# Performance work log

Hardware: AMD Instinct MI355X
Metric: run time of the kernel (lower is better)

Reference implementation:

```python
import jax, jax.numpy as jnp
import numpy as np

N_NODES = 80000
N_EDGES = 1280000
IN_CH = 128
HID = 64
N_GRAPHS = 64
DROPOUT_P = 0.3


def setup_inputs() -> dict:
    key = jax.random.key(0)
    ks = jax.random.split(key, 12)
    x = jax.random.normal(ks[0], (N_NODES, IN_CH), dtype=jnp.float32)
    edge_index = jax.random.randint(ks[1], (2, N_EDGES), 0, N_NODES, dtype=jnp.int64 if jax.config.read('jax_enable_x64') else jnp.int32)
    batch = jnp.sort(jax.random.randint(ks[2], (N_NODES,), 0, N_GRAPHS))
    def lin(k, fan_in, fan_out):
        lim = 1.0 / np.sqrt(fan_in)
        kw, kb = jax.random.split(k)
        W = jax.random.uniform(kw, (fan_in, fan_out), minval=-lim, maxval=lim, dtype=jnp.float32)
        b = jax.random.uniform(kb, (fan_out,), minval=-lim, maxval=lim, dtype=jnp.float32)
        return W, b
    W1, b1 = lin(ks[3], IN_CH, HID)
    W2, b2 = lin(ks[4], HID, HID)
    W3, b3 = lin(ks[5], HID, HID)
    Wm1, bm1 = lin(ks[6], HID, HID)
    Wm2, bm2 = lin(ks[7], HID, 1)
    return {"x": x, "edge_index": edge_index, "batch": batch,
            "W1": W1, "b1": b1, "W2": W2, "b2": b2, "W3": W3, "b3": b3,
            "Wm1": Wm1, "bm1": bm1, "Wm2": Wm2, "bm2": bm2}


def _gcn_conv(x, W, b, src, dst, deg_inv_sqrt):
    # PyG GCNConv: h = X W; add self-loops; norm_e = d^-1/2[src] * d^-1/2[dst]
    h = x @ W  # [N, F]
    norm = deg_inv_sqrt[src] * deg_inv_sqrt[dst]  # [E]
    agg = jax.ops.segment_sum(h[src] * norm[:, None], dst, num_segments=x.shape[0])
    agg = agg + h * (deg_inv_sqrt * deg_inv_sqrt)[:, None]  # self-loop term d^-1
    return agg + b


def _dropout(x, key, p):
    keep = jax.random.bernoulli(key, 1.0 - p, x.shape)
    return jnp.where(keep, x / (1.0 - p), 0.0)


def reference(x, edge_index, batch, W1, b1, W2, b2, W3, b3, Wm1, bm1, Wm2, bm2):
    src, dst = edge_index[0], edge_index[1]
    N = x.shape[0]
    # in-degree on dst, +1 for self-loop (PyG default normalization)
    deg = jax.ops.segment_sum(jnp.ones_like(dst, dtype=x.dtype), dst, num_segments=N) + 1.0
    deg_inv_sqrt = jax.lax.rsqrt(deg)

    dk = jax.random.split(jax.random.key(42), 4)
    h = _dropout(jax.nn.relu(_gcn_conv(x, W1, b1, src, dst, deg_inv_sqrt)), dk[0], DROPOUT_P)
    h = _dropout(jax.nn.relu(_gcn_conv(h, W2, b2, src, dst, deg_inv_sqrt)), dk[1], DROPOUT_P)
    h = _dropout(jax.nn.relu(_gcn_conv(h, W3, b3, src, dst, deg_inv_sqrt)), dk[2], DROPOUT_P)

    # global mean pool per graph
    sums = jax.ops.segment_sum(h, batch, num_segments=N_GRAPHS)
    counts = jax.ops.segment_sum(jnp.ones((N,), dtype=h.dtype), batch, num_segments=N_GRAPHS)
    pooled = sums / jnp.maximum(counts, 1.0)[:, None]  # [G, HID]

    # MLP head: Linear -> ReLU -> Dropout -> Linear
    m = jax.nn.relu(pooled @ Wm1 + bm1)
    m = _dropout(m, dk[3], DROPOUT_P)
    return m @ Wm2 + bm2  # [G, 1]
```

## Files before the change

kernel.cpp:

```cpp
#include <hip/hip_runtime.h>
#include <hip/hip_fp8.h>
#include <stdint.h>

#define HID 64
#define INCH 128
#define NGRAPH 64
#define KEEPP 0.7f
#define CAP 64
#define CAPSH 6

typedef __attribute__((ext_vector_type(8))) short short8;
typedef __attribute__((ext_vector_type(4))) float floatx4;

__device__ __forceinline__ uint8_t f2e4(float f) {
  __hip_fp8_e4m3 t(f);
  return (uint8_t)t.__x;
}
__device__ __forceinline__ float e42f(uint8_t b) {
  __hip_fp8_e4m3 t;
  t.__x = (__hip_fp8_storage_t)b;
  return (float)t;
}

__host__ __device__ inline void tf2x32(uint32_t k0, uint32_t k1,
                                       uint32_t& x0, uint32_t& x1) {
  const uint32_t ks2 = k0 ^ k1 ^ 0x1BD11BDAu;
#define ROTL32(v, d) (((v) << (d)) | ((v) >> (32 - (d))))
#define TF_RND(r) { x0 += x1; x1 = ROTL32(x1, r); x1 ^= x0; }
  x0 += k0; x1 += k1;
  TF_RND(13) TF_RND(15) TF_RND(26) TF_RND(6)
  x0 += k1;  x1 += ks2 + 1u;
  TF_RND(17) TF_RND(29) TF_RND(16) TF_RND(24)
  x0 += ks2; x1 += k0 + 2u;
  TF_RND(13) TF_RND(15) TF_RND(26) TF_RND(6)
  x0 += k0;  x1 += k1 + 3u;
  TF_RND(17) TF_RND(29) TF_RND(16) TF_RND(24)
  x0 += k1;  x1 += ks2 + 4u;
  TF_RND(13) TF_RND(15) TF_RND(26) TF_RND(6)
  x0 += ks2; x1 += k0 + 5u;
#undef TF_RND
#undef ROTL32
}

__device__ __forceinline__ bool keep_mask(uint32_t k0, uint32_t k1, uint32_t idx) {
  uint32_t x0 = 0u, x1 = idx;
  tf2x32(k0, k1, x0, x1);
  uint32_t bits = x0 ^ x1;
  float u = __uint_as_float((bits >> 9) | 0x3f800000u) - 1.0f;
  return u < KEEPP;
}

__device__ __forceinline__ void wsplit_one(const float* __restrict__ W,
                                           short8* __restrict__ Wh,
                                           short8* __restrict__ Wl, int i) {
  int lane = i & 63, f = i >> 6;
  int kc = f >> 2, ct = f & 3;
  int kbase = kc * 32 + ((lane >> 4) << 3);
  int n = ct * 16 + (lane & 15);
  short8 h, l;
#pragma unroll
  for (int j = 0; j < 8; ++j) {
    float w = W[(size_t)(kbase + j) * HID + n];
    uint32_t u = __float_as_uint(w);
    h[j] = (short)(u >> 16);
    float r = w - __uint_as_float(u & 0xFFFF0000u);
    l[j] = (short)(__float_as_uint(r) >> 16);
  }
  Wh[i] = h;
  Wl[i] = l;
}

__global__ __launch_bounds__(1024) void k_prep(
    const float* __restrict__ W1, short8* __restrict__ Wh1, short8* __restrict__ Wl1,
    const float* __restrict__ W2, short8* __restrict__ Wh2, short8* __restrict__ Wl2,
    const float* __restrict__ W3, short8* __restrict__ Wh3, short8* __restrict__ Wl3,
    int* __restrict__ counts, float* __restrict__ sums, float* __restrict__ cnts,
    int N) {
  const int b = blockIdx.x;
  const int tid = threadIdx.x;
  if (b == 0) {
    wsplit_one(W1, Wh1, Wl1, tid);
  } else if (b == 1) {
    if (tid < 512) wsplit_one(W2, Wh2, Wl2, tid);
  } else if (b == 2) {
    if (tid < 512) wsplit_one(W3, Wh3, Wl3, tid);
  } else {
    for (int i = tid; i < N; i += 1024) counts[i] = 0;
    for (int i = tid; i < NGRAPH * HID; i += 1024) sums[i] = 0.0f;
    if (tid < NGRAPH) cnts[tid] = 0.0f;
  }
}

template <int K>
__device__ __forceinline__ void mgemm_tile(const float* __restrict__ A,
                                           const short8* __restrict__ Wh,
                                           const short8* __restrict__ Wl,
                                           uint8_t* __restrict__ C, int N,
                                           int tile) {
  constexpr int KC = K / 32;
  const int lane = threadIdx.x & 63;
  const int wv = threadIdx.x >> 6;
  const int m = lane & 15;
  const int q = lane >> 4;
  const int row0 = tile * 64 + wv * 16;
  if (row0 >= N) return;
  const int arow = min(row0 + m, N - 1);
  const float* __restrict__ ap = A + (size_t)arow * K + (q << 3);

  floatx4 acc[4];
#pragma unroll
  for (int ct = 0; ct < 4; ++ct) acc[ct] = (floatx4){0.f, 0.f, 0.f, 0.f};

#pragma unroll
  for (int kc = 0; kc < KC; ++kc) {
    const floatx4* apv = (const floatx4*)(ap + kc * 32);
    floatx4 x0 = apv[0];
    floatx4 x1 = apv[1];
    short8 ah, al;
#pragma unroll
    for (int j = 0; j < 4; ++j) {
      uint32_t u = __float_as_uint(x0[j]);
      ah[j] = (short)(u >> 16);
      float r = x0[j] - __uint_as_float(u & 0xFFFF0000u);
      al[j] = (short)(__float_as_uint(r) >> 16);
    }
#pragma unroll
    for (int j = 0; j < 4; ++j) {
      uint32_t u = __float_as_uint(x1[j]);
      ah[4 + j] = (short)(u >> 16);
      float r = x1[j] - __uint_as_float(u & 0xFFFF0000u);
      al[4 + j] = (short)(__float_as_uint(r) >> 16);
    }
#pragma unroll
    for (int ct = 0; ct < 4; ++ct) {
      short8 bh = Wh[(kc * 4 + ct) * 64 + lane];
      short8 bl = Wl[(kc * 4 + ct) * 64 + lane];
      acc[ct] = __builtin_amdgcn_mfma_f32_16x16x32_bf16(ah, bh, acc[ct], 0, 0, 0);
      acc[ct] = __builtin_amdgcn_mfma_f32_16x16x32_bf16(ah, bl, acc[ct], 0, 0, 0);
      acc[ct] = __builtin_amdgcn_mfma_f32_16x16x32_bf16(al, bh, acc[ct], 0, 0, 0);
    }
  }

  uint8_t* __restrict__ cp = C + (size_t)row0 * HID;
#pragma unroll
  for (int ct = 0; ct < 4; ++ct)
#pragma unroll
    for (int r = 0; r < 4; ++r) {
      int rr = (q << 2) + r;
      if (row0 + rr < N) cp[(size_t)rr * HID + ct * 16 + m] = f2e4(acc[ct][r]);
    }
}

template <int K>
__global__ __launch_bounds__(256) void k_build_gemm(
    const float* __restrict__ A, const short8* __restrict__ Wh,
    const short8* __restrict__ Wl, uint8_t* __restrict__ C, int N,
    const int* __restrict__ src, const int* __restrict__ dst,
    int* __restrict__ counts, int* __restrict__ cap,
    int E, int build_blocks, int gemm_blocks) {
  const long T = (long)build_blocks + gemm_blocks;
  const long b = (long)blockIdx.x;
  const long gb = (b * gemm_blocks) / T;
  const bool is_g = (((b + 1) * gemm_blocks) / T) != gb;
  if (!is_g) {
    int bb = (int)(b - gb);
    int e = bb * 256 + (int)threadIdx.x;
    if (e < E) {
      int s = src[e], d = dst[e];
      int r = atomicAdd(&counts[d], 1);
      if (r < CAP) cap[(d << CAPSH) + r] = s;
    }
    return;
  }
  mgemm_tile<K>(A, Wh, Wl, C, N, (int)gb);
}

template <int K>
__global__ __launch_bounds__(256) void k_mgemm(const float* __restrict__ A,
                                               const short8* __restrict__ Wh,
                                               const short8* __restrict__ Wl,
                                               uint8_t* __restrict__ C, int N) {
  mgemm_tile<K>(A, Wh, Wl, C, N, (int)blockIdx.x);
}

__global__ __launch_bounds__(256) void k_gather(const uint8_t* __restrict__ tmp,
                                                const int* __restrict__ counts,
                                                const int* __restrict__ cap,
                                                const float* __restrict__ bias,
                                                float* __restrict__ outh, int N,
                                                uint32_t k0, uint32_t k1) {
  const int node = blockIdx.x * 4 + (threadIdx.x >> 6);
  const int lane = threadIdx.x & 63;
  if (node >= N) return;
  const int degn = __builtin_amdgcn_readfirstlane(counts[node]);
  const int deg = min(degn, CAP);
  const int base = node << CAPSH;
  float acc0 = 0.0f, acc1 = 0.0f, acc2 = 0.0f, acc3 = 0.0f;
  int j = 0;
  for (; j + 7 < deg; j += 8) {
    int4 e0 = *(const int4*)&cap[base + j];
    int4 e1 = *(const int4*)&cap[base + j + 4];
    int c0 = counts[e0.x], c1 = counts[e0.y], c2 = counts[e0.z], c3 = counts[e0.w];
    int c4 = counts[e1.x], c5 = counts[e1.y], c6 = counts[e1.z], c7 = counts[e1.w];
    float v0 = e42f(tmp[(size_t)e0.x * HID + lane]);
    float v1 = e42f(tmp[(size_t)e0.y * HID + lane]);
    float v2 = e42f(tmp[(size_t)e0.z * HID + lane]);
    float v3 = e42f(tmp[(size_t)e0.w * HID + lane]);
    float v4 = e42f(tmp[(size_t)e1.x * HID + lane]);
    float v5 = e42f(tmp[(size_t)e1.y * HID + lane]);
    float v6 = e42f(tmp[(size_t)e1.z * HID + lane]);
    float v7 = e42f(tmp[(size_t)e1.w * HID + lane]);
    acc0 = fmaf(v0, rsqrtf((float)c0 + 1.0f), acc0);
    acc1 = fmaf(v1, rsqrtf((float)c1 + 1.0f), acc1);
    acc2 = fmaf(v2, rsqrtf((float)c2 + 1.0f), acc2);
    acc3 = fmaf(v3, rsqrtf((float)c3 + 1.0f), acc3);
    acc0 = fmaf(v4, rsqrtf((float)c4 + 1.0f), acc0);
    acc1 = fmaf(v5, rsqrtf((float)c5 + 1.0f), acc1);
    acc2 = fmaf(v6, rsqrtf((float)c6 + 1.0f), acc2);
    acc3 = fmaf(v7, rsqrtf((float)c7 + 1.0f), acc3);
  }
  for (; j < deg; ++j) {
    int s = cap[base + j];
    float w = rsqrtf((float)counts[s] + 1.0f);
    acc2 = fmaf(e42f(tmp[(size_t)s * HID + lane]), w, acc2);
  }
  float acc = (acc0 + acc1) + (acc2 + acc3);
  const float dn = rsqrtf((float)degn + 1.0f);
  const int idx = node * HID + lane;
  float v = dn * (acc + e42f(tmp[idx]) * dn) + bias[lane];
  v = fmaxf(v, 0.0f);
  v = keep_mask(k0, k1, (uint32_t)idx) ? v / KEEPP : 0.0f;
  outh[idx] = v;
}

__global__ __launch_bounds__(256) void k_pool(const float* __restrict__ h,
                                              const int* __restrict__ batch,
                                              float* __restrict__ sums,
                                              float* __restrict__ cnts, int N) {
  __shared__ float ls[NGRAPH * HID];
  __shared__ float lc[NGRAPH];
  for (int i = threadIdx.x; i < NGRAPH * HID; i += 256) ls[i] = 0.0f;
  if (threadIdx.x < NGRAPH) lc[threadIdx.x] = 0.0f;
  __syncthreads();
  const int lane = threadIdx.x & 63;
  const int wave = threadIdx.x >> 6;
  int per = (N + gridDim.x - 1) / gridDim.x;
  int beg = blockIdx.x * per;
  int end = min(N, beg + per);
  for (int i = beg + wave; i < end; i += 4) {
    int g = batch[i];
    atomicAdd(&ls[g * HID + lane], h[(size_t)i * HID + lane]);
    if (lane == 0) atomicAdd(&lc[g], 1.0f);
  }
  __syncthreads();
  for (int i = threadIdx.x; i < NGRAPH * HID; i += 256)
    if (ls[i] != 0.0f) atomicAdd(&sums[i], ls[i]);
  if (threadIdx.x < NGRAPH && lc[threadIdx.x] != 0.0f)
    atomicAdd(&cnts[threadIdx.x], lc[threadIdx.x]);
}

__global__ __launch_bounds__(256) void k_head(const float* __restrict__ sums,
                                              const float* __restrict__ cnts,
                                              const float* __restrict__ Wm1,
                                              const float* __restrict__ bm1,
                                              const float* __restrict__ Wm2,
                                              const float* __restrict__ bm2,
                                              float* __restrict__ out,
                                              uint32_t k0, uint32_t k1) {
  __shared__ float pooled[NGRAPH * HID];
  __shared__ float m[NGRAPH * HID];
  for (int i = threadIdx.x; i < NGRAPH * HID; i += 256) {
    int g = i >> 6;
    pooled[i] = sums[i] / fmaxf(cnts[g], 1.0f);
  }
  __syncthreads();
  for (int i = threadIdx.x; i < NGRAPH * HID; i += 256) {
    int g = i >> 6, j = i & 63;
    float acc = bm1[j];
#pragma unroll 8
    for (int k = 0; k < HID; ++k)
      acc = fmaf(pooled[g * HID + k], Wm1[k * HID + j], acc);
    acc = fmaxf(acc, 0.0f);
    m[i] = keep_mask(k0, k1, (uint32_t)i) ? acc / KEEPP : 0.0f;
  }
  __syncthreads();
  if (threadIdx.x < NGRAPH) {
    int g = threadIdx.x;
    float acc = bm2[0];
#pragma unroll 8
    for (int j = 0; j < HID; ++j)
      acc = fmaf(m[g * HID + j], Wm2[j], acc);
    out[g] = acc;
  }
}

extern "C" void kernel_launch(void* const* d_in, const int* in_sizes, int n_in,
                              void* d_out, int out_size, void* d_ws, size_t ws_size,
                              hipStream_t stream) {
  const float* x     = (const float*)d_in[0];
  const int*   ei    = (const int*)d_in[1];
  const int*   batch = (const int*)d_in[2];
  const float* W1 = (const float*)d_in[3];
  const float* b1 = (const float*)d_in[4];
  const float* W2 = (const float*)d_in[5];
  const float* b2 = (const float*)d_in[6];
  const float* W3 = (const float*)d_in[7];
  const float* b3 = (const float*)d_in[8];
  const float* Wm1 = (const float*)d_in[9];
  const float* bm1 = (const float*)d_in[10];
  const float* Wm2 = (const float*)d_in[11];
  const float* bm2 = (const float*)d_in[12];
  float* out = (float*)d_out;

  const int N = in_sizes[0] / INCH;
  const int E = in_sizes[1] / 2;
  const int* src = ei;
  const int* dst = ei + E;

  char* ws = (char*)d_ws;
  size_t off = 0;
  uint8_t* B0 = (uint8_t*)(ws + off); off += (size_t)N * HID;
  off = (off + 15) & ~(size_t)15;
  float* B1     = (float*)(ws + off); off += (size_t)N * HID * 4;
  int*   counts = (int*)  (ws + off); off += (size_t)N * 4;
  int*   cap    = (int*)  (ws + off); off += (size_t)N * CAP * 4;
  float* sums   = (float*)(ws + off); off += NGRAPH * HID * 4;
  float* cnts   = (float*)(ws + off); off += NGRAPH * 4;
  off = (off + 15) & ~(size_t)15;
  short8* Wh1 = (short8*)(ws + off); off += 1024 * 16;
  short8* Wl1 = (short8*)(ws + off); off += 1024 * 16;
  short8* Wh2 = (short8*)(ws + off); off += 512 * 16;
  short8* Wl2 = (short8*)(ws + off); off += 512 * 16;
  short8* Wh3 = (short8*)(ws + off); off += 512 * 16;
  short8* Wl3 = (short8*)(ws + off); off += 512 * 16;

  uint32_t dk[4][2];
  for (uint32_t i = 0; i < 4; ++i) {
    uint32_t a = 0u, b = i;
    tf2x32(0u, 42u, a, b);
    dk[i][0] = a; dk[i][1] = b;
  }

  const int build_grid = (E + 255) / 256;
  const int mg_grid    = (N + 63) / 64;
  const int gath_grid  = (N + 3) / 4;

  k_prep<<<4, 1024, 0, stream>>>(W1, Wh1, Wl1, W2, Wh2, Wl2, W3, Wh3, Wl3,
                                 counts, sums, cnts, N);

  k_build_gemm<INCH><<<build_grid + mg_grid, 256, 0, stream>>>(
      x, Wh1, Wl1, B0, N, src, dst, counts, cap, E, build_grid, mg_grid);
  k_gather<<<gath_grid, 256, 0, stream>>>(B0, counts, cap, b1,
                                          B1, N, dk[0][0], dk[0][1]);
  k_mgemm<HID><<<mg_grid, 256, 0, stream>>>(B1, Wh2, Wl2, B0, N);
  k_gather<<<gath_grid, 256, 0, stream>>>(B0, counts, cap, b2,
                                          B1, N, dk[1][0], dk[1][1]);
  k_mgemm<HID><<<mg_grid, 256, 0, stream>>>(B1, Wh3, Wl3, B0, N);
  k_gather<<<gath_grid, 256, 0, stream>>>(B0, counts, cap, b3,
                                          B1, N, dk[2][0], dk[2][1]);

  k_pool<<<256, 256, 0, stream>>>(B1, batch, sums, cnts, N);
  k_head<<<1, 256, 0, stream>>>(sums, cnts, Wm1, bm1, Wm2, bm2, out,
                                dk[3][0], dk[3][1]);
  (void)n_in; (void)out_size; (void)ws_size;
}
```

Measured before the change: 421.2 us.

## Pre-scale GEMM output by source degree norm to drop per-edge count loads

Result: faster. 407.9 us (-3.2%).

```diff
diff --git a/kernel.cpp b/kernel.cpp
--- a/kernel.cpp
+++ b/kernel.cpp
@@ -91,18 +91,31 @@
   }
 }
 
+__global__ __launch_bounds__(256) void k_build(const int* __restrict__ src,
+                                               const int* __restrict__ dst,
+                                               int* __restrict__ counts,
+                                               int* __restrict__ cap, int E) {
+  int e = blockIdx.x * 256 + threadIdx.x;
+  if (e < E) {
+    int s = src[e], d = dst[e];
+    int r = atomicAdd(&counts[d], 1);
+    if (r < CAP) cap[(d << CAPSH) + r] = s;
+  }
+}
+
 template <int K>
-__device__ __forceinline__ void mgemm_tile(const float* __restrict__ A,
-                                           const short8* __restrict__ Wh,
-                                           const short8* __restrict__ Wl,
-                                           uint8_t* __restrict__ C, int N,
-                                           int tile) {
+__global__ __launch_bounds__(256) void k_mgemm_s(const float* __restrict__ A,
+                                                 const short8* __restrict__ Wh,
+                                                 const short8* __restrict__ Wl,
+                                                 uint8_t* __restrict__ C,
+                                                 const int* __restrict__ counts,
+                                                 int N) {
   constexpr int KC = K / 32;
   const int lane = threadIdx.x & 63;
   const int wv = threadIdx.x >> 6;
   const int m = lane & 15;
   const int q = lane >> 4;
-  const int row0 = tile * 64 + wv * 16;
+  const int row0 = (int)blockIdx.x * 64 + wv * 16;
   if (row0 >= N) return;
   const int arow = min(row0 + m, N - 1);
   const float* __restrict__ ap = A + (size_t)arow * K + (q << 3);
@@ -141,54 +154,29 @@
     }
   }
 
+  float dv[4];
+#pragma unroll
+  for (int r = 0; r < 4; ++r) {
+    int gr = min(row0 + (q << 2) + r, N - 1);
+    dv[r] = rsqrtf((float)counts[gr] + 1.0f);
+  }
+
   uint8_t* __restrict__ cp = C + (size_t)row0 * HID;
 #pragma unroll
   for (int ct = 0; ct < 4; ++ct)
 #pragma unroll
     for (int r = 0; r < 4; ++r) {
       int rr = (q << 2) + r;
-      if (row0 + rr < N) cp[(size_t)rr * HID + ct * 16 + m] = f2e4(acc[ct][r]);
+      if (row0 + rr < N) cp[(size_t)rr * HID + ct * 16 + m] = f2e4(acc[ct][r] * dv[r]);
     }
 }
 
-template <int K>
-__global__ __launch_bounds__(256) void k_build_gemm(
-    const float* __restrict__ A, const short8* __restrict__ Wh,
-    const short8* __restrict__ Wl, uint8_t* __restrict__ C, int N,
-    const int* __restrict__ src, const int* __restrict__ dst,
-    int* __restrict__ counts, int* __restrict__ cap,
-    int E, int build_blocks, int gemm_blocks) {
-  const long T = (long)build_blocks + gemm_blocks;
-  const long b = (long)blockIdx.x;
-  const long gb = (b * gemm_blocks) / T;
-  const bool is_g = (((b + 1) * gemm_blocks) / T) != gb;
-  if (!is_g) {
-    int bb = (int)(b - gb);
-    int e = bb * 256 + (int)threadIdx.x;
-    if (e < E) {
-      int s = src[e], d = dst[e];
-      int r = atomicAdd(&counts[d], 1);
-      if (r < CAP) cap[(d << CAPSH) + r] = s;
-    }
-    return;
-  }
-  mgemm_tile<K>(A, Wh, Wl, C, N, (int)gb);
-}
-
-template <int K>
-__global__ __launch_bounds__(256) void k_mgemm(const float* __restrict__ A,
-                                               const short8* __restrict__ Wh,
-                                               const short8* __restrict__ Wl,
-                                               uint8_t* __restrict__ C, int N) {
-  mgemm_tile<K>(A, Wh, Wl, C, N, (int)blockIdx.x);
-}
-
-__global__ __launch_bounds__(256) void k_gather(const uint8_t* __restrict__ tmp,
-                                                const int* __restrict__ counts,
-                                                const int* __restrict__ cap,
-                                                const float* __restrict__ bias,
-                                                float* __restrict__ outh, int N,
-                                                uint32_t k0, uint32_t k1) {
+__global__ __launch_bounds__(256) void k_gather_s(const uint8_t* __restrict__ tmp,
+                                                  const int* __restrict__ counts,
+                                                  const int* __restrict__ cap,
+                                                  const float* __restrict__ bias,
+                                                  float* __restrict__ outh, int N,
+                                                  uint32_t k0, uint32_t k1) {
   const int node = blockIdx.x * 4 + (threadIdx.x >> 6);
   const int lane = threadIdx.x & 63;
   if (node >= N) return;
@@ -200,8 +188,6 @@
   for (; j + 7 < deg; j += 8) {
     int4 e0 = *(const int4*)&cap[base + j];
     int4 e1 = *(const int4*)&cap[base + j + 4];
-    int c0 = counts[e0.x], c1 = counts[e0.y], c2 = counts[e0.z], c3 = counts[e0.w];
-    int c4 = counts[e1.x], c5 = counts[e1.y], c6 = counts[e1.z], c7 = counts[e1.w];
     float v0 = e42f(tmp[(size_t)e0.x * HID + lane]);
     float v1 = e42f(tmp[(size_t)e0.y * HID + lane]);
     float v2 = e42f(tmp[(size_t)e0.z * HID + lane]);
@@ -210,24 +196,22 @@
     float v5 = e42f(tmp[(size_t)e1.y * HID + lane]);
     float v6 = e42f(tmp[(size_t)e1.z * HID + lane]);
     float v7 = e42f(tmp[(size_t)e1.w * HID + lane]);
-    acc0 = fmaf(v0, rsqrtf((float)c0 + 1.0f), acc0);
-    acc1 = fmaf(v1, rsqrtf((float)c1 + 1.0f), acc1);
-    acc2 = fmaf(v2, rsqrtf((float)c2 + 1.0f), acc2);
-    acc3 = fmaf(v3, rsqrtf((float)c3 + 1.0f), acc3);
-    acc0 = fmaf(v4, rsqrtf((float)c4 + 1.0f), acc0);
-    acc1 = fmaf(v5, rsqrtf((float)c5 + 1.0f), acc1);
-    acc2 = fmaf(v6, rsqrtf((float)c6 + 1.0f), acc2);
-    acc3 = fmaf(v7, rsqrtf((float)c7 + 1.0f), acc3);
-  }
-  for (; j < deg; ++j) {
+    acc0 += v0; acc1 += v1; acc2 += v2; acc3 += v3;
+    acc0 += v4; acc1 += v5; acc2 += v6; acc3 += v7;
+  }
+  for (; j + 1 < deg; j += 2) {
+    int2 p = *(const int2*)&cap[base + j];
+    acc0 += e42f(tmp[(size_t)p.x * HID + lane]);
+    acc1 += e42f(tmp[(size_t)p.y * HID + lane]);
+  }
+  if (j < deg) {
     int s = cap[base + j];
-    float w = rsqrtf((float)counts[s] + 1.0f);
-    acc2 = fmaf(e42f(tmp[(size_t)s * HID + lane]), w, acc2);
+    acc2 += e42f(tmp[(size_t)s * HID + lane]);
   }
   float acc = (acc0 + acc1) + (acc2 + acc3);
   const float dn = rsqrtf((float)degn + 1.0f);
   const int idx = node * HID + lane;
-  float v = dn * (acc + e42f(tmp[idx]) * dn) + bias[lane];
+  float v = dn * (acc + e42f(tmp[idx])) + bias[lane];
   v = fmaxf(v, 0.0f);
   v = keep_mask(k0, k1, (uint32_t)idx) ? v / KEEPP : 0.0f;
   outh[idx] = v;
@@ -347,17 +331,17 @@
 
   k_prep<<<4, 1024, 0, stream>>>(W1, Wh1, Wl1, W2, Wh2, Wl2, W3, Wh3, Wl3,
                                  counts, sums, cnts, N);
-
-  k_build_gemm<INCH><<<build_grid + mg_grid, 256, 0, stream>>>(
-      x, Wh1, Wl1, B0, N, src, dst, counts, cap, E, build_grid, mg_grid);
-  k_gather<<<gath_grid, 256, 0, stream>>>(B0, counts, cap, b1,
-                                          B1, N, dk[0][0], dk[0][1]);
-  k_mgemm<HID><<<mg_grid, 256, 0, stream>>>(B1, Wh2, Wl2, B0, N);
-  k_gather<<<gath_grid, 256, 0, stream>>>(B0, counts, cap, b2,
-                                          B1, N, dk[1][0], dk[1][1]);
-  k_mgemm<HID><<<mg_grid, 256, 0, stream>>>(B1, Wh3, Wl3, B0, N);
-  k_gather<<<gath_grid, 256, 0, stream>>>(B0, counts, cap, b3,
-                                          B1, N, dk[2][0], dk[2][1]);
+  k_build<<<build_grid, 256, 0, stream>>>(src, dst, counts, cap, E);
+
+  k_mgemm_s<INCH><<<mg_grid, 256, 0, stream>>>(x, Wh1, Wl1, B0, counts, N);
+  k_gather_s<<<gath_grid, 256, 0, stream>>>(B0, counts, cap, b1,
+                                            B1, N, dk[0][0], dk[0][1]);
+  k_mgemm_s<HID><<<mg_grid, 256, 0, stream>>>(B1, Wh2, Wl2, B0, counts, N);
+  k_gather_s<<<gath_grid, 256, 0, stream>>>(B0, counts, cap, b2,
+                                            B1, N, dk[1][0], dk[1][1]);
+  k_mgemm_s<HID><<<mg_grid, 256, 0, stream>>>(B1, Wh3, Wl3, B0, counts, N);
+  k_gather_s<<<gath_grid, 256, 0, stream>>>(B0, counts, cap, b3,
+                                            B1, N, dk[2][0], dk[2][1]);
 
   k_pool<<<256, 256, 0, stream>>>(B1, batch, sums, cnts, N);
   k_head<<<1, 256, 0, stream>>>(sums, cnts, Wm1, bm1, Wm2, bm2, out,
```
